# Performance work log

Hardware: AMD Instinct MI355X
Metric: run time of the kernel (lower is better)

## Reference

```python
import jax, jax.numpy as jnp
import numpy as np

B, N, C, F = 8, 3, 64, 128
H = W = 128


def _up2(x):
    # nearest-neighbor upsample by 2 on the last two axes
    return jnp.repeat(jnp.repeat(x, 2, axis=-2), 2, axis=-1)


def setup_inputs() -> dict:
    key = jax.random.key(0)
    ks = jax.random.split(key, 12)
    s = lambda k, shp, fan: jax.random.normal(k, shp, jnp.float32) * (1.0 / np.sqrt(fan))
    return {
        "contexts": jax.random.normal(ks[0], (B, N, C, H, W), jnp.float32),
        "mainstream": jax.random.normal(ks[1], (B, F, H // 2, W // 2), jnp.float32),
        "Wc": s(ks[2], (C, C), C),        # W_context 1x1 conv weight [out,in]
        "bc": jnp.zeros((C,), jnp.float32),
        "Wf": s(ks[3], (C, F), F),        # W_feat 1x1
        "bf": jnp.zeros((C,), jnp.float32),
        "Wk": s(ks[4], (C, F), F),        # W_key_feat 1x1
        "bk": jnp.zeros((C,), jnp.float32),
        "Vw": s(ks[5], (C, F, 3, 3), F * 9),  # values_conv 3x3, OIHW
        "Vb": jnp.zeros((C,), jnp.float32),
    }


def reference(contexts, mainstream, Wc, bc, Wf, bf, Wk, bk, Vw, Vb):
    # contexts: [B,N,C,H,W], mainstream: [B,F,h,w]
    bias = lambda b: b[None, :, None, None]
    queries = jnp.einsum('bfhw,cf->bchw', mainstream, Wf) + bias(bf)       # [B,C,h,w]
    keys_m = jnp.einsum('bfhw,cf->bchw', mainstream, Wk) + bias(bk)        # [B,C,h,w]
    values = jax.lax.conv_general_dilated(
        mainstream, Vw, (1, 1), 'SAME',
        dimension_numbers=('NCHW', 'OIHW', 'NCHW')) + bias(Vb)             # [B,C,h,w]

    # stack contexts with upsampled mainstream keys, project with W_context (1x1)
    keys_stack = jnp.concatenate([contexts, _up2(keys_m)[:, None]], axis=1)  # [B,N+1,C,H,W]
    keys_proj = jnp.einsum('bnchw,dc->bndhw', keys_stack, Wc) + bc[None, None, :, None, None]

    q_up = _up2(queries)                                                    # [B,C,H,W]
    logits = jnp.einsum('bnchw,bchw->bnhw', keys_proj, q_up)                # [B,N+1,H,W]
    attn = jax.nn.softmax(logits, axis=1)                                   # softmax over contexts

    vals_stack = jnp.concatenate([contexts, _up2(values)[:, None]], axis=1) # [B,N+1,C,H,W]
    out = jnp.einsum('bnchw,bnhw->bchw', vals_stack, attn)                  # [B,C,H,W]
    return out
```

## Files before the change

### kernel.cpp

```cpp
#include <hip/hip_runtime.h>
#include <math.h>

#define CH   64
#define FD   128
#define HS   64
#define FS   128
#define NB   8
#define NCTX 3

#define WS_QT   0
#define WS_VAL  2097152
#define WS_L3   4194304
#define WS_BQ   4227072
#define WS_AVH  4227136
#define WS_AVL  4264000
#define WS_AQH  4300864
#define WS_AQL  4304960
#define WS_AKH  4309056
#define WS_AKL  4313152
#define WS_MTH  4317248
#define WS_MTL  6547520

#define MT2_IDX(b,row,kf,col,kh) \
  ((((((size_t)(b)*66+(row))*8+(kf))*66+(col))*2+(kh))*8)

typedef short  s16x8  __attribute__((ext_vector_type(8)));
typedef float  f32x16 __attribute__((ext_vector_type(16)));

__device__ inline unsigned short bf16_rne(float x) {
  unsigned u = __float_as_uint(x);
  u += 0x7FFFu + ((u >> 16) & 1u);
  return (unsigned short)(u >> 16);
}
__device__ inline void split2(float x, unsigned short& h, unsigned short& l) {
  h = bf16_rne(x);
  l = bf16_rne(x - __uint_as_float((unsigned)h << 16));
}

__global__ __launch_bounds__(256) void setup_all(
    const float* __restrict__ Wc, const float* __restrict__ Wf,
    const float* __restrict__ bf, const float* __restrict__ Wk,
    const float* __restrict__ Vw, const float* __restrict__ m,
    float* __restrict__ ws) {
  if (blockIdx.x < 45) {
    int id = blockIdx.x * 256 + threadIdx.x;
    unsigned short* avh = (unsigned short*)(ws + WS_AVH);
    unsigned short* aqh = (unsigned short*)(ws + WS_AQH);
    unsigned short* aql = (unsigned short*)(ws + WS_AQL);
    unsigned short* akh = (unsigned short*)(ws + WS_AKH);
    unsigned short* akl = (unsigned short*)(ws + WS_AKL);

    if (id < 9216) {
      int tile = id / 4608, rem = id % 4608;
      int q = rem >> 6, l = rem & 63;
      int am = l & 31, kh = l >> 5;
      int c = tile * 32 + am, tap = q >> 3, kf = q & 7;
#pragma unroll
      for (int j = 0; j < 8; ++j) {
        int f = kf * 16 + kh * 8 + j;
        avh[id * 8 + j] = bf16_rne(Vw[(c * FD + f) * 9 + tap]);
      }
    } else if (id < 10240) {
      int i2 = id - 9216;
      int tile = i2 >> 9, rem = i2 & 511;
      int q = rem >> 6, l = rem & 63;
      int am = l & 31, kh = l >> 5;
      int c = tile * 32 + am;
#pragma unroll
      for (int j = 0; j < 8; ++j) {
        int f = q * 16 + kh * 8 + j;
        float acc = 0.f;
        for (int d = 0; d < CH; ++d)
          acc = fmaf(Wc[d * CH + c], Wf[d * FD + f], acc);
        unsigned short h, lo; split2(acc, h, lo);
        aqh[i2 * 8 + j] = h; aql[i2 * 8 + j] = lo;
      }
    } else if (id < 11264) {
      int i3 = id - 10240;
      int tile = i3 >> 9, rem = i3 & 511;
      int q = rem >> 6, l = rem & 63;
      int am = l & 31, kh = l >> 5;
      int c = tile * 32 + am;
#pragma unroll
      for (int j = 0; j < 8; ++j) {
        int f = q * 16 + kh * 8 + j;
        unsigned short h, lo; split2(Wk[c * FD + f], h, lo);
        akh[i3 * 8 + j] = h; akl[i3 * 8 + j] = lo;
      }
    } else if (id < 11328) {
      int c = id - 11264;
      float acc = 0.f;
      for (int d = 0; d < CH; ++d) acc = fmaf(Wc[d * CH + c], bf[d], acc);
      ws[WS_BQ + c] = acc;
    }
  } else {
    unsigned short* mth = (unsigned short*)(ws + WS_MTH);
    unsigned short* mtl = (unsigned short*)(ws + WS_MTL);
    const int bid = blockIdx.x - 45;
    const int b = bid / 66, yp = bid % 66;
    const int lane = threadIdx.x & 63;
    const int wave = threadIdx.x >> 6;
    const int yy = yp - 1;
    const bool rowok = (yy >= 0) && (yy < HS);
#pragma unroll
    for (int cc = 0; cc < 4; ++cc) {
      const int f0 = wave * 32 + cc * 8;
      const int kf = f0 >> 4, kh = (f0 >> 3) & 1;
      float v[8];
      if (rowok) {
#pragma unroll
        for (int j = 0; j < 8; ++j)
          v[j] = m[((b * FD + f0 + j) * HS + yy) * HS + lane];
      } else {
#pragma unroll
        for (int j = 0; j < 8; ++j) v[j] = 0.f;
      }
      s16x8 hi, lo;
#pragma unroll
      for (int j = 0; j < 8; ++j) {
        unsigned short h, l; split2(v[j], h, l);
        hi[j] = (short)h; lo[j] = (short)l;
      }
      size_t base = MT2_IDX(b, yp, kf, lane + 1, kh);
      *(s16x8*)(mth + base) = hi;
      *(s16x8*)(mtl + base) = lo;
      if (lane < 2) {
        s16x8 z;
#pragma unroll
        for (int j = 0; j < 8; ++j) z[j] = 0;
        size_t bb = MT2_IDX(b, yp, kf, lane * 65, kh);
        *(s16x8*)(mth + bb) = z;
        *(s16x8*)(mtl + bb) = z;
      }
    }
  }
}

__global__ __launch_bounds__(1024, 8) void main_mfma(
    const unsigned short* __restrict__ mth, const unsigned short* __restrict__ mtl,
    const float* __restrict__ Vb, const float* __restrict__ bk,
    float* __restrict__ ws) {
  const int b = blockIdx.x >> 6, y = blockIdx.x & 63;
  const int t = threadIdx.x, lane = t & 63;
  const int wave = __builtin_amdgcn_readfirstlane(t >> 6);
  const int am = lane & 31, kh = lane >> 5;
  const int tile = wave & 3;
  const int x0 = (tile & 1) * 32, ch0 = (tile >> 1) * 32;
  const int ct = tile >> 1;
  const int khalf = wave >> 2;

  const unsigned short* avh = (const unsigned short*)(ws + WS_AVH);

  __shared__ float red[3][4][16][64];
  __shared__ float qtb[2][64][32];
  __shared__ float keb[2][64][32];

  f32x16 a1;
#pragma unroll
  for (int i = 0; i < 16; ++i) a1[i] = 0.f;
#pragma unroll 6
  for (int qi = 0; qi < 18; ++qi) {
    const int q = khalf * 18 + qi;
    const int tap = q >> 3, kf = q & 7;
    const s16x8 ah = *(const s16x8*)(avh + ((ct * 72 + q) * 64 + lane) * 8);
    const s16x8 bh = *(const s16x8*)(mth +
        MT2_IDX(b, y + tap / 3, kf, x0 + am + tap % 3, kh));
    a1 = __builtin_amdgcn_mfma_f32_32x32x16_bf16(ah, bh, a1, 0, 0, 0);
  }
  if (khalf) {
#pragma unroll
    for (int r = 0; r < 16; ++r) red[khalf - 1][tile][r][lane] = a1[r];
  }
  __syncthreads();
  if (!khalf) {
#pragma unroll
    for (int r = 0; r < 16; ++r) {
      const int c = ch0 + (r & 3) + 8 * (r >> 2) + 4 * kh;
      float v = a1[r] + red[0][tile][r][lane] + red[1][tile][r][lane]
              + red[2][tile][r][lane] + Vb[c];
      ws[WS_VAL + ((b * CH + c) * HS + y) * HS + x0 + am] = v;
    }
  }

  if (khalf < 2) {
    const unsigned short* Ah = (const unsigned short*)(ws + (khalf ? WS_AKH : WS_AQH));
    const unsigned short* Al = (const unsigned short*)(ws + (khalf ? WS_AKL : WS_AQL));
    f32x16 c1, c2;
#pragma unroll
    for (int i = 0; i < 16; ++i) { c1[i] = 0.f; c2[i] = 0.f; }
#pragma unroll
    for (int q = 0; q < 8; ++q) {
      const s16x8 ah = *(const s16x8*)(Ah + ((ct * 8 + q) * 64 + lane) * 8);
      const s16x8 al = *(const s16x8*)(Al + ((ct * 8 + q) * 64 + lane) * 8);
      const size_t base = MT2_IDX(b, y + 1, q, x0 + am + 1, kh);
      const s16x8 bh = *(const s16x8*)(mth + base);
      const s16x8 bl = *(const s16x8*)(mtl + base);
      c1 = __builtin_amdgcn_mfma_f32_32x32x16_bf16(ah, bh, c1, 0, 0, 0);
      c1 = __builtin_amdgcn_mfma_f32_32x32x16_bf16(al, bh, c1, 0, 0, 0);
      c2 = __builtin_amdgcn_mfma_f32_32x32x16_bf16(ah, bl, c2, 0, 0, 0);
    }
    const int ptile = tile & 1;
#pragma unroll
    for (int r = 0; r < 16; ++r) {
      const int c = ch0 + (r & 3) + 8 * (r >> 2) + 4 * kh;
      if (khalf) {
        keb[ptile][c][am] = c1[r] + c2[r] + bk[c];
      } else {
        float v = c1[r] + c2[r] + ws[WS_BQ + c];
        qtb[ptile][c][am] = v;
        ws[WS_QT + ((b * CH + c) * HS + y) * HS + x0 + am] = v;
      }
    }
  }
  __syncthreads();

  if (wave < 2) {
    float s = 0.f;
#pragma unroll 8
    for (int j = 0; j < 32; ++j)
      s = fmaf(qtb[wave][kh * 32 + j][am], keb[wave][kh * 32 + j][am], s);
    s += __shfl_xor(s, 32, 64);
    if (kh == 0)
      ws[WS_L3 + (b * HS + y) * HS + wave * 32 + am] = s;
  }
}

__global__ __launch_bounds__(256) void fullres_kernel(
    const float* __restrict__ ctx, const float* __restrict__ ws,
    float* __restrict__ out) {
  const int xh = blockIdx.x & 1, hrow = blockIdx.x >> 1;
  const int b = blockIdx.y;
  const int quad = threadIdx.x & 15;
  const int cg = threadIdx.x >> 4;
  const int x = xh * 64 + quad * 4;
  const int h2 = hrow >> 1, w2 = (x >> 1);
  const int c0 = cg * 4;

  const size_t cbase = (size_t)(b * NCTX * CH) * FS * FS + hrow * FS + x;
  const int cs = FS * FS, ns = CH * FS * FS;

  float4 cv[3][4];
  float2 qv[4];
#pragma unroll
  for (int j = 0; j < 4; ++j) {
    const int c = c0 + j;
    cv[0][j] = *(const float4*)(ctx + cbase + c * cs);
    cv[1][j] = *(const float4*)(ctx + cbase + ns + c * cs);
    cv[2][j] = *(const float4*)(ctx + cbase + 2 * ns + c * cs);
    qv[j] = *(const float2*)(ws + WS_QT + (size_t)(b * CH + c) * HS * HS + h2 * HS + w2);
  }

  float4 pl[3];
#pragma unroll
  for (int n = 0; n < 3; ++n) {
    pl[n].x = pl[n].y = pl[n].z = pl[n].w = 0.f;
#pragma unroll
    for (int j = 0; j < 4; ++j) {
      pl[n].x = fmaf(cv[n][j].x, qv[j].x, pl[n].x);
      pl[n].y = fmaf(cv[n][j].y, qv[j].x, pl[n].y);
      pl[n].z = fmaf(cv[n][j].z, qv[j].y, pl[n].z);
      pl[n].w = fmaf(cv[n][j].w, qv[j].y, pl[n].w);
    }
  }

  __shared__ float4 part[3][16][17];
  __shared__ float  Lred[3][64];
#pragma unroll
  for (int n = 0; n < 3; ++n) part[n][cg][quad] = pl[n];
  __syncthreads();

  {
    const int tt = threadIdx.x;
    if (tt < 192) {
      const int n = tt >> 6, px = tt & 63;
      const float* pp = (const float*)part + (size_t)n * 16 * 17 * 4 + px;
      float s = 0.f;
#pragma unroll
      for (int g = 0; g < 16; ++g) s += pp[g * 68];
      Lred[n][px] = s;
    }
  }
  __syncthreads();

  float4 Lv0 = *(const float4*)&Lred[0][quad * 4];
  float4 Lv1 = *(const float4*)&Lred[1][quad * 4];
  float4 Lv2 = *(const float4*)&Lred[2][quad * 4];
  float2 l3v = *(const float2*)(ws + WS_L3 + (b * HS + h2) * HS + w2);

  float A0[4], A1[4], A2[4], A3[4];
  const float* L0p = (const float*)&Lv0;
  const float* L1p = (const float*)&Lv1;
  const float* L2p = (const float*)&Lv2;
#pragma unroll
  for (int k = 0; k < 4; ++k) {
    float L0 = L0p[k], L1 = L1p[k], L2 = L2p[k];
    float L3 = (k < 2) ? l3v.x : l3v.y;
    float mx = fmaxf(fmaxf(L0, L1), fmaxf(L2, L3));
    float e0 = __expf(L0 - mx), e1 = __expf(L1 - mx);
    float e2 = __expf(L2 - mx), e3 = __expf(L3 - mx);
    float inv = 1.f / (e0 + e1 + e2 + e3);
    A0[k] = e0 * inv; A1[k] = e1 * inv; A2[k] = e2 * inv; A3[k] = e3 * inv;
  }

  float* op = out + (size_t)(b * CH) * FS * FS + hrow * FS + x;
#pragma unroll
  for (int j = 0; j < 4; ++j) {
    const int c = c0 + j;
    float2 vv = *(const float2*)(ws + WS_VAL + (size_t)(b * CH + c) * HS * HS + h2 * HS + w2);
    float4 o;
    o.x = fmaf(A0[0], cv[0][j].x, fmaf(A1[0], cv[1][j].x, fmaf(A2[0], cv[2][j].x, A3[0] * vv.x)));
    o.y = fmaf(A0[1], cv[0][j].y, fmaf(A1[1], cv[1][j].y, fmaf(A2[1], cv[2][j].y, A3[1] * vv.x)));
    o.z = fmaf(A0[2], cv[0][j].z, fmaf(A1[2], cv[1][j].z, fmaf(A2[2], cv[2][j].z, A3[2] * vv.y)));
    o.w = fmaf(A0[3], cv[0][j].w, fmaf(A1[3], cv[1][j].w, fmaf(A2[3], cv[2][j].w, A3[3] * vv.y)));
    *(float4*)(op + c * cs) = o;
  }
}

extern "C" void kernel_launch(void* const* d_in, const int* in_sizes, int n_in,
                              void* d_out, int out_size, void* d_ws, size_t ws_size,
                              hipStream_t stream) {
  const float* ctx = (const float*)d_in[0];
  const float* ms  = (const float*)d_in[1];
  const float* Wc  = (const float*)d_in[2];
  const float* Wf  = (const float*)d_in[4];
  const float* bf  = (const float*)d_in[5];
  const float* Wk  = (const float*)d_in[6];
  const float* bk  = (const float*)d_in[7];
  const float* Vw  = (const float*)d_in[8];
  const float* Vb  = (const float*)d_in[9];
  float* ws  = (float*)d_ws;
  float* out = (float*)d_out;

  unsigned short* mth = (unsigned short*)(ws + WS_MTH);
  unsigned short* mtl = (unsigned short*)(ws + WS_MTL);

  setup_all<<<45 + NB * 66, 256, 0, stream>>>(Wc, Wf, bf, Wk, Vw, ms, ws);
  main_mfma<<<NB * HS, 1024, 0, stream>>>(mth, mtl, Vb, bk, ws);
  fullres_kernel<<<dim3(2 * FS, NB), 256, 0, stream>>>(ctx, ws, out);
}
```

Baseline: 252.9 us.

## Fuse mainstream bf16 staging into MFMA kernel via LDS halo tile

Removes the global padded hi/lo mainstream buffers. The MFMA kernel now builds the three-row bf16 halo tile in shared memory directly from the fp32 input, and computes the low part on the fly for the query/key 1x1 projections. Waves are reorganised: four waves run the full 72-step 3x3 conv without cross-wave reduction, and four run query and key together, reducing the logit term in registers. This saves a large global write and read round trip and a split-K LDS reduction, at the cost of redundant per-row input loads (three rows per block) and longer conv chains per wave.

```diff
diff --git a/kernel.cpp b/kernel.cpp
--- a/kernel.cpp
+++ b/kernel.cpp
@@ -13,16 +13,10 @@
 #define WS_L3   4194304
 #define WS_BQ   4227072
 #define WS_AVH  4227136
-#define WS_AVL  4264000
-#define WS_AQH  4300864
-#define WS_AQL  4304960
-#define WS_AKH  4309056
-#define WS_AKL  4313152
-#define WS_MTH  4317248
-#define WS_MTL  6547520
-
-#define MT2_IDX(b,row,kf,col,kh) \
-  ((((((size_t)(b)*66+(row))*8+(kf))*66+(col))*2+(kh))*8)
+#define WS_AQH  4264000
+#define WS_AQL  4268096
+#define WS_AKH  4272192
+#define WS_AKL  4276288
 
 typedef short  s16x8  __attribute__((ext_vector_type(8)));
 typedef float  f32x16 __attribute__((ext_vector_type(16)));
@@ -37,191 +31,171 @@
   l = bf16_rne(x - __uint_as_float((unsigned)h << 16));
 }
 
-__global__ __launch_bounds__(256) void setup_all(
+__global__ __launch_bounds__(256) void afrag_prep(
     const float* __restrict__ Wc, const float* __restrict__ Wf,
     const float* __restrict__ bf, const float* __restrict__ Wk,
-    const float* __restrict__ Vw, const float* __restrict__ m,
-    float* __restrict__ ws) {
-  if (blockIdx.x < 45) {
-    int id = blockIdx.x * 256 + threadIdx.x;
-    unsigned short* avh = (unsigned short*)(ws + WS_AVH);
-    unsigned short* aqh = (unsigned short*)(ws + WS_AQH);
-    unsigned short* aql = (unsigned short*)(ws + WS_AQL);
-    unsigned short* akh = (unsigned short*)(ws + WS_AKH);
-    unsigned short* akl = (unsigned short*)(ws + WS_AKL);
-
-    if (id < 9216) {
-      int tile = id / 4608, rem = id % 4608;
-      int q = rem >> 6, l = rem & 63;
-      int am = l & 31, kh = l >> 5;
-      int c = tile * 32 + am, tap = q >> 3, kf = q & 7;
-#pragma unroll
-      for (int j = 0; j < 8; ++j) {
-        int f = kf * 16 + kh * 8 + j;
-        avh[id * 8 + j] = bf16_rne(Vw[(c * FD + f) * 9 + tap]);
-      }
-    } else if (id < 10240) {
-      int i2 = id - 9216;
-      int tile = i2 >> 9, rem = i2 & 511;
-      int q = rem >> 6, l = rem & 63;
-      int am = l & 31, kh = l >> 5;
-      int c = tile * 32 + am;
-#pragma unroll
-      for (int j = 0; j < 8; ++j) {
-        int f = q * 16 + kh * 8 + j;
-        float acc = 0.f;
-        for (int d = 0; d < CH; ++d)
-          acc = fmaf(Wc[d * CH + c], Wf[d * FD + f], acc);
-        unsigned short h, lo; split2(acc, h, lo);
-        aqh[i2 * 8 + j] = h; aql[i2 * 8 + j] = lo;
-      }
-    } else if (id < 11264) {
-      int i3 = id - 10240;
-      int tile = i3 >> 9, rem = i3 & 511;
-      int q = rem >> 6, l = rem & 63;
-      int am = l & 31, kh = l >> 5;
-      int c = tile * 32 + am;
-#pragma unroll
-      for (int j = 0; j < 8; ++j) {
-        int f = q * 16 + kh * 8 + j;
-        unsigned short h, lo; split2(Wk[c * FD + f], h, lo);
-        akh[i3 * 8 + j] = h; akl[i3 * 8 + j] = lo;
-      }
-    } else if (id < 11328) {
-      int c = id - 11264;
+    const float* __restrict__ Vw, float* __restrict__ ws) {
+  int id = blockIdx.x * 256 + threadIdx.x;
+  unsigned short* avh = (unsigned short*)(ws + WS_AVH);
+  unsigned short* aqh = (unsigned short*)(ws + WS_AQH);
+  unsigned short* aql = (unsigned short*)(ws + WS_AQL);
+  unsigned short* akh = (unsigned short*)(ws + WS_AKH);
+  unsigned short* akl = (unsigned short*)(ws + WS_AKL);
+
+  if (id < 9216) {
+    int tile = id / 4608, rem = id % 4608;
+    int q = rem >> 6, l = rem & 63;
+    int am = l & 31, kh = l >> 5;
+    int c = tile * 32 + am, tap = q >> 3, kf = q & 7;
+#pragma unroll
+    for (int j = 0; j < 8; ++j) {
+      int f = kf * 16 + kh * 8 + j;
+      avh[id * 8 + j] = bf16_rne(Vw[(c * FD + f) * 9 + tap]);
+    }
+  } else if (id < 10240) {
+    int i2 = id - 9216;
+    int tile = i2 >> 9, rem = i2 & 511;
+    int q = rem >> 6, l = rem & 63;
+    int am = l & 31, kh = l >> 5;
+    int c = tile * 32 + am;
+#pragma unroll
+    for (int j = 0; j < 8; ++j) {
+      int f = q * 16 + kh * 8 + j;
       float acc = 0.f;
-      for (int d = 0; d < CH; ++d) acc = fmaf(Wc[d * CH + c], bf[d], acc);
-      ws[WS_BQ + c] = acc;
-    }
-  } else {
-    unsigned short* mth = (unsigned short*)(ws + WS_MTH);
-    unsigned short* mtl = (unsigned short*)(ws + WS_MTL);
-    const int bid = blockIdx.x - 45;
-    const int b = bid / 66, yp = bid % 66;
-    const int lane = threadIdx.x & 63;
-    const int wave = threadIdx.x >> 6;
-    const int yy = yp - 1;
-    const bool rowok = (yy >= 0) && (yy < HS);
-#pragma unroll
-    for (int cc = 0; cc < 4; ++cc) {
-      const int f0 = wave * 32 + cc * 8;
-      const int kf = f0 >> 4, kh = (f0 >> 3) & 1;
-      float v[8];
-      if (rowok) {
-#pragma unroll
-        for (int j = 0; j < 8; ++j)
-          v[j] = m[((b * FD + f0 + j) * HS + yy) * HS + lane];
-      } else {
-#pragma unroll
-        for (int j = 0; j < 8; ++j) v[j] = 0.f;
-      }
-      s16x8 hi, lo;
-#pragma unroll
-      for (int j = 0; j < 8; ++j) {
-        unsigned short h, l; split2(v[j], h, l);
-        hi[j] = (short)h; lo[j] = (short)l;
-      }
-      size_t base = MT2_IDX(b, yp, kf, lane + 1, kh);
-      *(s16x8*)(mth + base) = hi;
-      *(s16x8*)(mtl + base) = lo;
-      if (lane < 2) {
-        s16x8 z;
-#pragma unroll
-        for (int j = 0; j < 8; ++j) z[j] = 0;
-        size_t bb = MT2_IDX(b, yp, kf, lane * 65, kh);
-        *(s16x8*)(mth + bb) = z;
-        *(s16x8*)(mtl + bb) = z;
-      }
-    }
-  }
-}
-
-__global__ __launch_bounds__(1024, 8) void main_mfma(
-    const unsigned short* __restrict__ mth, const unsigned short* __restrict__ mtl,
-    const float* __restrict__ Vb, const float* __restrict__ bk,
-    float* __restrict__ ws) {
+      for (int d = 0; d < CH; ++d)
+        acc = fmaf(Wc[d * CH + c], Wf[d * FD + f], acc);
+      unsigned short h, lo; split2(acc, h, lo);
+      aqh[i2 * 8 + j] = h; aql[i2 * 8 + j] = lo;
+    }
+  } else if (id < 11264) {
+    int i3 = id - 10240;
+    int tile = i3 >> 9, rem = i3 & 511;
+    int q = rem >> 6, l = rem & 63;
+    int am = l & 31, kh = l >> 5;
+    int c = tile * 32 + am;
+#pragma unroll
+    for (int j = 0; j < 8; ++j) {
+      int f = q * 16 + kh * 8 + j;
+      unsigned short h, lo; split2(Wk[c * FD + f], h, lo);
+      akh[i3 * 8 + j] = h; akl[i3 * 8 + j] = lo;
+    }
+  } else if (id < 11328) {
+    int c = id - 11264;
+    float acc = 0.f;
+    for (int d = 0; d < CH; ++d) acc = fmaf(Wc[d * CH + c], bf[d], acc);
+    ws[WS_BQ + c] = acc;
+  }
+}
+
+__global__ __launch_bounds__(512) void half_fused(
+    const float* __restrict__ m, const float* __restrict__ Vb,
+    const float* __restrict__ bk, float* __restrict__ ws) {
   const int b = blockIdx.x >> 6, y = blockIdx.x & 63;
   const int t = threadIdx.x, lane = t & 63;
   const int wave = __builtin_amdgcn_readfirstlane(t >> 6);
   const int am = lane & 31, kh = lane >> 5;
-  const int tile = wave & 3;
-  const int x0 = (tile & 1) * 32, ch0 = (tile >> 1) * 32;
-  const int ct = tile >> 1;
-  const int khalf = wave >> 2;
-
-  const unsigned short* avh = (const unsigned short*)(ws + WS_AVH);
-
-  __shared__ float red[3][4][16][64];
-  __shared__ float qtb[2][64][32];
-  __shared__ float keb[2][64][32];
-
-  f32x16 a1;
-#pragma unroll
-  for (int i = 0; i < 16; ++i) a1[i] = 0.f;
-#pragma unroll 6
-  for (int qi = 0; qi < 18; ++qi) {
-    const int q = khalf * 18 + qi;
-    const int tap = q >> 3, kf = q & 7;
-    const s16x8 ah = *(const s16x8*)(avh + ((ct * 72 + q) * 64 + lane) * 8);
-    const s16x8 bh = *(const s16x8*)(mth +
-        MT2_IDX(b, y + tap / 3, kf, x0 + am + tap % 3, kh));
-    a1 = __builtin_amdgcn_mfma_f32_32x32x16_bf16(ah, bh, a1, 0, 0, 0);
-  }
-  if (khalf) {
-#pragma unroll
-    for (int r = 0; r < 16; ++r) red[khalf - 1][tile][r][lane] = a1[r];
+
+  __shared__ __align__(16) short HI[3][8][66][2][8];
+  __shared__ float l3red[2][64];
+
+  if (t < 96) {
+    int row = t / 32, kf = (t >> 2) & 7, khh = (t >> 1) & 1, col = (t & 1) * 65;
+    s16x8 z;
+#pragma unroll
+    for (int j = 0; j < 8; ++j) z[j] = 0;
+    *(s16x8*)&HI[row][kf][col][khh][0] = z;
+  }
+
+#pragma unroll
+  for (int i = 0; i < 6; ++i) {
+    const int tk = wave * 6 + i;
+    const int row = tk >> 4, kf = (tk >> 1) & 7, khh = tk & 1;
+    const int yy = y + row - 1;
+    s16x8 hi;
+    if (yy >= 0 && yy < HS) {
+#pragma unroll
+      for (int j = 0; j < 8; ++j) {
+        const int f = kf * 16 + khh * 8 + j;
+        hi[j] = (short)bf16_rne(m[((b * FD + f) * HS + yy) * HS + lane]);
+      }
+    } else {
+#pragma unroll
+      for (int j = 0; j < 8; ++j) hi[j] = 0;
+    }
+    *(s16x8*)&HI[row][kf][lane + 1][khh][0] = hi;
   }
   __syncthreads();
-  if (!khalf) {
+
+  float l3part = 0.f;
+  if (wave < 4) {
+    const int ct = wave >> 1, xh = wave & 1;
+    const int x0 = xh * 32, ch0 = ct * 32;
+    const unsigned short* avh = (const unsigned short*)(ws + WS_AVH);
+    f32x16 acc;
+#pragma unroll
+    for (int i = 0; i < 16; ++i) acc[i] = 0.f;
+#pragma unroll 8
+    for (int q = 0; q < 72; ++q) {
+      const int tap = q >> 3, kf = q & 7;
+      const s16x8 ah = *(const s16x8*)(avh + ((ct * 72 + q) * 64 + lane) * 8);
+      const s16x8 bh = *(const s16x8*)&HI[tap / 3][kf][x0 + am + tap % 3][kh][0];
+      acc = __builtin_amdgcn_mfma_f32_32x32x16_bf16(ah, bh, acc, 0, 0, 0);
+    }
 #pragma unroll
     for (int r = 0; r < 16; ++r) {
       const int c = ch0 + (r & 3) + 8 * (r >> 2) + 4 * kh;
-      float v = a1[r] + red[0][tile][r][lane] + red[1][tile][r][lane]
-              + red[2][tile][r][lane] + Vb[c];
-      ws[WS_VAL + ((b * CH + c) * HS + y) * HS + x0 + am] = v;
-    }
-  }
-
-  if (khalf < 2) {
-    const unsigned short* Ah = (const unsigned short*)(ws + (khalf ? WS_AKH : WS_AQH));
-    const unsigned short* Al = (const unsigned short*)(ws + (khalf ? WS_AKL : WS_AQL));
-    f32x16 c1, c2;
-#pragma unroll
-    for (int i = 0; i < 16; ++i) { c1[i] = 0.f; c2[i] = 0.f; }
+      ws[WS_VAL + ((b * CH + c) * HS + y) * HS + x0 + am] = acc[r] + Vb[c];
+    }
+  } else {
+    const int w4 = wave - 4;
+    const int ct = w4 >> 1, xh = w4 & 1;
+    const int x0 = xh * 32, ch0 = ct * 32;
+    const unsigned short* aqh = (const unsigned short*)(ws + WS_AQH);
+    const unsigned short* aql = (const unsigned short*)(ws + WS_AQL);
+    const unsigned short* akh = (const unsigned short*)(ws + WS_AKH);
+    const unsigned short* akl = (const unsigned short*)(ws + WS_AKL);
+    f32x16 q1, q2, k1, k2;
+#pragma unroll
+    for (int i = 0; i < 16; ++i) { q1[i] = 0.f; q2[i] = 0.f; k1[i] = 0.f; k2[i] = 0.f; }
 #pragma unroll
     for (int q = 0; q < 8; ++q) {
-      const s16x8 ah = *(const s16x8*)(Ah + ((ct * 8 + q) * 64 + lane) * 8);
-      const s16x8 al = *(const s16x8*)(Al + ((ct * 8 + q) * 64 + lane) * 8);
-      const size_t base = MT2_IDX(b, y + 1, q, x0 + am + 1, kh);
-      const s16x8 bh = *(const s16x8*)(mth + base);
-      const s16x8 bl = *(const s16x8*)(mtl + base);
-      c1 = __builtin_amdgcn_mfma_f32_32x32x16_bf16(ah, bh, c1, 0, 0, 0);
-      c1 = __builtin_amdgcn_mfma_f32_32x32x16_bf16(al, bh, c1, 0, 0, 0);
-      c2 = __builtin_amdgcn_mfma_f32_32x32x16_bf16(ah, bl, c2, 0, 0, 0);
-    }
-    const int ptile = tile & 1;
+      const s16x8 bh = *(const s16x8*)&HI[1][q][x0 + am + 1][kh][0];
+      s16x8 bl;
+#pragma unroll
+      for (int j = 0; j < 8; ++j) {
+        const float mv = m[((b * FD + q * 16 + kh * 8 + j) * HS + y) * HS + x0 + am];
+        const float hf = __uint_as_float(((unsigned)(unsigned short)bh[j]) << 16);
+        bl[j] = (short)bf16_rne(mv - hf);
+      }
+      const s16x8 ah = *(const s16x8*)(aqh + ((ct * 8 + q) * 64 + lane) * 8);
+      const s16x8 al = *(const s16x8*)(aql + ((ct * 8 + q) * 64 + lane) * 8);
+      const s16x8 kah = *(const s16x8*)(akh + ((ct * 8 + q) * 64 + lane) * 8);
+      const s16x8 kal = *(const s16x8*)(akl + ((ct * 8 + q) * 64 + lane) * 8);
+      q1 = __builtin_amdgcn_mfma_f32_32x32x16_bf16(ah, bh, q1, 0, 0, 0);
+      q1 = __builtin_amdgcn_mfma_f32_32x32x16_bf16(al, bh, q1, 0, 0, 0);
+      q2 = __builtin_amdgcn_mfma_f32_32x32x16_bf16(ah, bl, q2, 0, 0, 0);
+      k1 = __builtin_amdgcn_mfma_f32_32x32x16_bf16(kah, bh, k1, 0, 0, 0);
+      k1 = __builtin_amdgcn_mfma_f32_32x32x16_bf16(kal, bh, k1, 0, 0, 0);
+      k2 = __builtin_amdgcn_mfma_f32_32x32x16_bf16(kah, bl, k2, 0, 0, 0);
+    }
 #pragma unroll
     for (int r = 0; r < 16; ++r) {
       const int c = ch0 + (r & 3) + 8 * (r >> 2) + 4 * kh;
-      if (khalf) {
-        keb[ptile][c][am] = c1[r] + c2[r] + bk[c];
-      } else {
-        float v = c1[r] + c2[r] + ws[WS_BQ + c];
-        qtb[ptile][c][am] = v;
-        ws[WS_QT + ((b * CH + c) * HS + y) * HS + x0 + am] = v;
-      }
-    }
+      const float qv = q1[r] + q2[r] + ws[WS_BQ + c];
+      const float kv = k1[r] + k2[r] + bk[c];
+      ws[WS_QT + ((b * CH + c) * HS + y) * HS + x0 + am] = qv;
+      l3part = fmaf(qv, kv, l3part);
+    }
+    if (ct == 1) l3red[xh][lane] = l3part;
   }
   __syncthreads();
 
-  if (wave < 2) {
-    float s = 0.f;
-#pragma unroll 8
-    for (int j = 0; j < 32; ++j)
-      s = fmaf(qtb[wave][kh * 32 + j][am], keb[wave][kh * 32 + j][am], s);
+  if (wave == 4 || wave == 5) {
+    const int xh = wave - 4;
+    float s = l3part + l3red[xh][lane];
     s += __shfl_xor(s, 32, 64);
     if (kh == 0)
-      ws[WS_L3 + (b * HS + y) * HS + wave * 32 + am] = s;
+      ws[WS_L3 + (b * HS + y) * HS + xh * 32 + am] = s;
   }
 }
 
@@ -331,10 +305,7 @@
   float* ws  = (float*)d_ws;
   float* out = (float*)d_out;
 
-  unsigned short* mth = (unsigned short*)(ws + WS_MTH);
-  unsigned short* mtl = (unsigned short*)(ws + WS_MTL);
-
-  setup_all<<<45 + NB * 66, 256, 0, stream>>>(Wc, Wf, bf, Wk, Vw, ms, ws);
-  main_mfma<<<NB * HS, 1024, 0, stream>>>(mth, mtl, Vb, bk, ws);
+  afrag_prep<<<45, 256, 0, stream>>>(Wc, Wf, bf, Wk, Vw, ws);
+  half_fused<<<NB * HS, 512, 0, stream>>>(ms, Vb, bk, ws);
   fullres_kernel<<<dim3(2 * FS, NB), 256, 0, stream>>>(ctx, ws, out);
 }
```

Result: faster. 247.8 us (-2.0%).
